# Performance work log

Measured on AMD Instinct MI355X. Metric: run time of the kernel, lower is better.

Reference implementation:

```python
import jax, jax.numpy as jnp
import numpy as np

N_NODES = 50000
N_EDGES = 800000
N_REL = 8
OUT_CH = 64      # latent dim of z
HID = 128        # hidden_channels
IN_CH = 128      # reconstructed feature dim
NEG_SLOPE = 0.2


def rgat_conv(x, src, dst, edge_type, weight, q, k, bias, num_nodes):
    """PyG RGATConv, heads=1, dim=1, additive-self-attention, across-relation.
    x: [N, in]; weight: [R, in, out]; q,k: [out, 1]; bias: [out]."""
    # per-relation transform of all nodes, then per-edge gather (same math as
    # per-edge bmm with weight[edge_type], avoids [E, in, out] intermediate)
    x_all = jnp.einsum('ni,rio->nro', x, weight)          # [N, R, out]
    x_j = x_all[src, edge_type]                            # [E, out]
    x_i = x_all[dst, edge_type]                            # [E, out]
    alpha = (x_i @ q + x_j @ k)[:, 0]                      # [E]
    alpha = jax.nn.leaky_relu(alpha, NEG_SLOPE)
    # scatter-softmax over destination neighborhoods
    m = jax.ops.segment_max(alpha, dst, num_segments=num_nodes)
    m = jnp.where(jnp.isfinite(m), m, 0.0)                 # empty segments -> 0
    ex = jnp.exp(alpha - m[dst])
    denom = jax.ops.segment_sum(ex, dst, num_segments=num_nodes)
    a = ex / (denom[dst] + 1e-16)                          # [E]
    out = jax.ops.segment_sum(a[:, None] * x_j, dst, num_segments=num_nodes)
    return out + bias


def setup_inputs() -> dict:
    key = jax.random.key(0)
    ks = jax.random.split(key, 12)
    z = jax.random.normal(ks[0], (N_NODES, OUT_CH), dtype=jnp.float32)
    edge_index = jax.random.randint(ks[1], (2, N_EDGES), 0, N_NODES, dtype=jnp.int32)
    edge_type = jax.random.randint(ks[2], (N_EDGES,), 0, N_REL, dtype=jnp.int32)

    def glorot(k_, shape):
        fan = shape[-2] + shape[-1]
        return jax.random.normal(k_, shape, dtype=jnp.float32) * jnp.sqrt(2.0 / fan)

    return {
        'z': z,
        'lin_w': glorot(ks[3], (HID, OUT_CH)),
        'lin_b': jnp.zeros((HID,), dtype=jnp.float32),
        'w1': glorot(ks[4], (N_REL, HID, HID)),
        'q1': glorot(ks[5], (HID, 1)),
        'k1': glorot(ks[6], (HID, 1)),
        'b1': jnp.zeros((HID,), dtype=jnp.float32),
        'w2': glorot(ks[7], (N_REL, HID, IN_CH)),
        'q2': glorot(ks[8], (IN_CH, 1)),
        'k2': glorot(ks[9], (IN_CH, 1)),
        'b2': jnp.zeros((IN_CH,), dtype=jnp.float32),
        'edge_index': edge_index,
        'edge_type': edge_type,
    }


def reference(z, lin_w, lin_b, w1, q1, k1, b1, w2, q2, k2, b2, edge_index, edge_type):
    num_nodes = z.shape[0]
    src, dst = edge_index[0], edge_index[1]
    h = z @ lin_w.T + lin_b                                 # nn.Linear
    h = jax.nn.relu(rgat_conv(h, src, dst, edge_type, w1, q1, k1, b1, num_nodes))
    # dropout is identity in eval mode
    recon_x = rgat_conv(h, src, dst, edge_type, w2, q2, k2, b2, num_nodes)
    return recon_x
```

## Files before the change

### kernel.cpp

```cpp
#include <hip/hip_runtime.h>
#include <hip/hip_bf16.h>
#include <cstdint>
#include <cstddef>

#define N_NODES 50000
#define N_EDGES 800000
#define NSEG    (N_NODES * 8)

using frag_t = __attribute__((ext_vector_type(8))) short;
using f32x4  = __attribute__((ext_vector_type(4))) float;

__device__ __forceinline__ short f2bf(float x) {
    __hip_bfloat16 h = __float2bfloat16(x);
    return *reinterpret_cast<short*>(&h);
}
__device__ __forceinline__ float bf2f(unsigned int u) {
    union { unsigned int i; float f; } v;
    v.i = u << 16;
    return v.f;
}
__device__ __forceinline__ unsigned int packbf2(float lo, float hi) {
    unsigned int a = (unsigned short)f2bf(lo);
    unsigned int b = (unsigned short)f2bf(hi);
    return a | (b << 16);
}


__global__ void hist_kernel(const int* __restrict__ dst, const int* __restrict__ et,
                            int* __restrict__ deg8, int E) {
    int e = blockIdx.x * 256 + threadIdx.x;
    if (e < E) atomicAdd(&deg8[dst[e] * 8 + et[e]], 1);
}

__global__ __launch_bounds__(256) void scan_part(const int* __restrict__ deg8,
                                                 int* __restrict__ part, int M) {
    __shared__ int red[256];
    int t = threadIdx.x;
    int idx = blockIdx.x * 1024 + t * 4;
    int s = 0;
    if (idx + 3 < M) {
        int4 d = *(const int4*)(deg8 + idx);
        s = d.x + d.y + d.z + d.w;
    } else {
        for (int c = 0; c < 4; c++) if (idx + c < M) s += deg8[idx + c];
    }
    red[t] = s;
    __syncthreads();
    #pragma unroll
    for (int off = 128; off; off >>= 1) {
        if (t < off) red[t] += red[t + off];
        __syncthreads();
    }
    if (t == 0) part[blockIdx.x] = red[0];
}

__global__ __launch_bounds__(512) void scan_mid(int* __restrict__ part, int nparts,
                                                int* __restrict__ rowp, int M) {
    __shared__ int buf[512];
    int t = threadIdx.x;
    int own = (t < nparts) ? part[t] : 0;
    buf[t] = own;
    __syncthreads();
    for (int off = 1; off < 512; off <<= 1) {
        int v = buf[t];
        int u = (t >= off) ? buf[t - off] : 0;
        __syncthreads();
        buf[t] = v + u;
        __syncthreads();
    }
    if (t < nparts) part[t] = buf[t] - own;
    if (t == 511) rowp[M] = buf[511];
}

__global__ __launch_bounds__(256) void scan_fix(const int* __restrict__ deg8,
                                                const int* __restrict__ part,
                                                int* __restrict__ rowp,
                                                int* __restrict__ cursor, int M) {
    __shared__ int wsum[4];
    int t = threadIdx.x, lane = t & 63, w = t >> 6;
    int idx = blockIdx.x * 1024 + t * 4;
    int v0 = 0, v1 = 0, v2 = 0, v3 = 0;
    if (idx + 3 < M) {
        int4 d = *(const int4*)(deg8 + idx);
        v0 = d.x; v1 = d.y; v2 = d.z; v3 = d.w;
    } else {
        if (idx     < M) v0 = deg8[idx];
        if (idx + 1 < M) v1 = deg8[idx + 1];
        if (idx + 2 < M) v2 = deg8[idx + 2];
        if (idx + 3 < M) v3 = deg8[idx + 3];
    }
    int tsum = v0 + v1 + v2 + v3;
    int sc = tsum;
    #pragma unroll
    for (int off = 1; off < 64; off <<= 1) {
        int u = __shfl_up(sc, off, 64);
        if (lane >= off) sc += u;
    }
    if (lane == 63) wsum[w] = sc;
    __syncthreads();
    int woff = 0;
    for (int i = 0; i < w; i++) woff += wsum[i];
    int excl = part[blockIdx.x] + woff + sc - tsum;
    if (idx     < M) { rowp[idx]     = excl; cursor[idx]     = excl; } excl += v0;
    if (idx + 1 < M) { rowp[idx + 1] = excl; cursor[idx + 1] = excl; } excl += v1;
    if (idx + 2 < M) { rowp[idx + 2] = excl; cursor[idx + 2] = excl; } excl += v2;
    if (idx + 3 < M) { rowp[idx + 3] = excl; cursor[idx + 3] = excl; }
}

__global__ void fill_kernel(const int* __restrict__ src, const int* __restrict__ dst,
                            const int* __restrict__ et, int* __restrict__ cursor,
                            int* __restrict__ sorted, int E) {
    int e = blockIdx.x * 256 + threadIdx.x;
    if (e < E) {
        int pos = atomicAdd(&cursor[dst[e] * 8 + et[e]], 1);
        sorted[pos] = src[e] | (et[e] << 16);
    }
}


__global__ __launch_bounds__(256) void gemm_lin(const float* __restrict__ A,
                                                const float* __restrict__ B,
                                                const float* __restrict__ bias,
                                                unsigned short* __restrict__ hb, int N) {
    const int Kdim = 64;
    __shared__ float As[32][64];
    __shared__ float Bs[32][128];
    int t = threadIdx.x;
    int n0 = blockIdx.x * 64;
    int rg = t >> 4, cg = t & 15;
    int an = t >> 2, ak = (t & 3) * 8;
    float acc[4][8] = {};

    for (int k0 = 0; k0 < Kdim; k0 += 32) {
        int gn = n0 + an;
        if (gn < N) {
            const float* ap = A + (size_t)gn * Kdim + k0 + ak;
            float4 v0 = *(const float4*)ap;
            float4 v1 = *(const float4*)(ap + 4);
            As[ak + 0][an] = v0.x; As[ak + 1][an] = v0.y;
            As[ak + 2][an] = v0.z; As[ak + 3][an] = v0.w;
            As[ak + 4][an] = v1.x; As[ak + 5][an] = v1.y;
            As[ak + 6][an] = v1.z; As[ak + 7][an] = v1.w;
        } else {
            #pragma unroll
            for (int c = 0; c < 8; c++) As[ak + c][an] = 0.f;
        }
        {
            int o = t >> 1, kh = (t & 1) * 16;
            const float* bp = B + (size_t)o * Kdim + k0 + kh;
            #pragma unroll
            for (int j = 0; j < 4; j++) {
                float4 v = ((const float4*)bp)[j];
                Bs[kh + j * 4 + 0][o] = v.x;
                Bs[kh + j * 4 + 1][o] = v.y;
                Bs[kh + j * 4 + 2][o] = v.z;
                Bs[kh + j * 4 + 3][o] = v.w;
            }
        }
        __syncthreads();
        #pragma unroll
        for (int k = 0; k < 32; k++) {
            float a[4], b[8];
            *(float4*)&a[0] = *(const float4*)&As[k][rg * 4];
            *(float4*)&b[0] = *(const float4*)&Bs[k][cg * 8];
            *(float4*)&b[4] = *(const float4*)&Bs[k][cg * 8 + 4];
            #pragma unroll
            for (int i = 0; i < 4; i++)
                #pragma unroll
                for (int j = 0; j < 8; j++)
                    acc[i][j] = fmaf(a[i], b[j], acc[i][j]);
        }
        __syncthreads();
    }
    #pragma unroll
    for (int i = 0; i < 4; i++) {
        int gn = n0 + rg * 4 + i;
        if (gn < N) {
            unsigned short us[8];
            #pragma unroll
            for (int j = 0; j < 8; j++)
                us[j] = (unsigned short)f2bf(acc[i][j] + bias[cg * 8 + j]);
            *(int4*)(hb + (size_t)gn * 128 + cg * 8) = *(int4*)&us[0];
        }
    }
}


__global__ void wconv_kernel(const float* __restrict__ W, short* __restrict__ Bf) {
    int idx = blockIdx.x * 256 + threadIdx.x;
    int k = idx >> 7, o = idx & 127;
    float v = W[(size_t)k * 128 + o];
    Bf[(((size_t)(k >> 3) * 128) + o) * 8 + (k & 7)] = f2bf(v);
}


__global__ void wqk_kernel(const float* __restrict__ W, const float* __restrict__ q,
                           const float* __restrict__ k, float* __restrict__ wq,
                           float* __restrict__ wk) {
    int g = blockIdx.x * 256 + threadIdx.x;
    int which = g >> 10;
    int r = (g >> 7) & 7;
    int i = g & 127;
    const float* vec = which ? k : q;
    const float* wrow = W + ((size_t)r * 128 + i) * 128;
    float acc = 0.f;
    #pragma unroll 4
    for (int o = 0; o < 128; o++) acc = fmaf(wrow[o], vec[o], acc);
    (which ? wk : wq)[r * 128 + i] = acc;
}


__global__ __launch_bounds__(256) void qk_table_kernel(const unsigned short* __restrict__ xb,
                                                       const float* __restrict__ wq,
                                                       const float* __restrict__ wk,
                                                       float* __restrict__ Q,
                                                       float* __restrict__ K, int N) {
    int n = blockIdx.x * 256 + threadIdx.x;
    if (n >= N) return;
    const uint2* row = (const uint2*)(xb + (size_t)n * 128);
    float aq[8] = {}, ak[8] = {};
    for (int i = 0; i < 32; i++) {
        uint2 d = row[i];
        float x0 = bf2f(d.x & 0xFFFFu);
        float x1 = bf2f(d.x >> 16);
        float x2 = bf2f(d.y & 0xFFFFu);
        float x3 = bf2f(d.y >> 16);
        int c = i * 4;
        #pragma unroll
        for (int r = 0; r < 8; r++) {
            const float* wqr = wq + r * 128 + c;
            const float* wkr = wk + r * 128 + c;
            aq[r] = fmaf(x0, wqr[0], fmaf(x1, wqr[1], fmaf(x2, wqr[2], fmaf(x3, wqr[3], aq[r]))));
            ak[r] = fmaf(x0, wkr[0], fmaf(x1, wkr[1], fmaf(x2, wkr[2], fmaf(x3, wkr[3], ak[r]))));
        }
    }
    float4* qp = (float4*)(Q + (size_t)n * 8);
    qp[0] = *(float4*)&aq[0];
    qp[1] = *(float4*)&aq[4];
    float4* kp = (float4*)(K + (size_t)n * 8);
    kp[0] = *(float4*)&ak[0];
    kp[1] = *(float4*)&ak[4];
}


__global__ __launch_bounds__(256) void agg_s_kernel(const unsigned short* __restrict__ hb,
                                                    const float* __restrict__ Q,
                                                    const float* __restrict__ Kt,
                                                    const int* __restrict__ rowp8,
                                                    const int* __restrict__ sorted,
                                                    short* __restrict__ s, int N) {
    int wv = threadIdx.x >> 6;
    int lane = threadIdx.x & 63;
    int n = blockIdx.x * 4 + wv;
    if (n >= N) return;
    int beg = rowp8[n * 8];
    int end = rowp8[n * 8 + 8];
    int deg = end - beg;
    unsigned int* spw = (unsigned int*)(s + (size_t)n * 1024);
    const unsigned int* hbu = (const unsigned int*)hb;

    if (deg == 0) {
        int4 z = {0, 0, 0, 0};
        int4* p = (int4*)spw;
        p[lane * 2]     = z;
        p[lane * 2 + 1] = z;
        return;
    }

    float2 acc = {0.f, 0.f};
    int rcur = 0;

    if (deg <= 64) {
        int pk = 0;
        float a = -INFINITY;
        if (lane < deg) {
            pk = sorted[beg + lane];
            int srcn = pk & 0xFFFF, etj = pk >> 16;
            a = Q[(size_t)n * 8 + etj] + Kt[(size_t)srcn * 8 + etj];
            a = (a > 0.f) ? a : 0.2f * a;
        }
        float m = a;
        #pragma unroll
        for (int off = 32; off; off >>= 1) m = fmaxf(m, __shfl_xor(m, off, 64));
        float e = (lane < deg) ? __expf(a - m) : 0.f;
        float sum = e;
        #pragma unroll
        for (int off = 32; off; off >>= 1) sum += __shfl_xor(sum, off, 64);
        float w = e / (sum + 1e-16f);

        int j = 0;
        for (; j + 4 <= deg; j += 4) {
            int   p0 = __shfl(pk, j, 64),     p1 = __shfl(pk, j + 1, 64);
            int   p2 = __shfl(pk, j + 2, 64), p3 = __shfl(pk, j + 3, 64);
            float w0 = __shfl(w, j, 64),      w1 = __shfl(w, j + 1, 64);
            float w2 = __shfl(w, j + 2, 64),  w3 = __shfl(w, j + 3, 64);
            unsigned int d0 = hbu[(size_t)(p0 & 0xFFFF) * 64 + lane];
            unsigned int d1 = hbu[(size_t)(p1 & 0xFFFF) * 64 + lane];
            unsigned int d2 = hbu[(size_t)(p2 & 0xFFFF) * 64 + lane];
            unsigned int d3 = hbu[(size_t)(p3 & 0xFFFF) * 64 + lane];
            int e0 = p0 >> 16, e1 = p1 >> 16, e2 = p2 >> 16, e3 = p3 >> 16;
            while (rcur < e0) { spw[rcur * 64 + lane] = packbf2(acc.x, acc.y); acc.x = acc.y = 0.f; rcur++; }
            acc.x = fmaf(w0, bf2f(d0 & 0xFFFF), acc.x); acc.y = fmaf(w0, bf2f(d0 >> 16), acc.y);
            while (rcur < e1) { spw[rcur * 64 + lane] = packbf2(acc.x, acc.y); acc.x = acc.y = 0.f; rcur++; }
            acc.x = fmaf(w1, bf2f(d1 & 0xFFFF), acc.x); acc.y = fmaf(w1, bf2f(d1 >> 16), acc.y);
            while (rcur < e2) { spw[rcur * 64 + lane] = packbf2(acc.x, acc.y); acc.x = acc.y = 0.f; rcur++; }
            acc.x = fmaf(w2, bf2f(d2 & 0xFFFF), acc.x); acc.y = fmaf(w2, bf2f(d2 >> 16), acc.y);
            while (rcur < e3) { spw[rcur * 64 + lane] = packbf2(acc.x, acc.y); acc.x = acc.y = 0.f; rcur++; }
            acc.x = fmaf(w3, bf2f(d3 & 0xFFFF), acc.x); acc.y = fmaf(w3, bf2f(d3 >> 16), acc.y);
        }
        for (; j < deg; j++) {
            int   p0 = __shfl(pk, j, 64);
            float w0 = __shfl(w, j, 64);
            unsigned int d0 = hbu[(size_t)(p0 & 0xFFFF) * 64 + lane];
            int e0 = p0 >> 16;
            while (rcur < e0) { spw[rcur * 64 + lane] = packbf2(acc.x, acc.y); acc.x = acc.y = 0.f; rcur++; }
            acc.x = fmaf(w0, bf2f(d0 & 0xFFFF), acc.x); acc.y = fmaf(w0, bf2f(d0 >> 16), acc.y);
        }
        while (rcur < 8) { spw[rcur * 64 + lane] = packbf2(acc.x, acc.y); acc.x = acc.y = 0.f; rcur++; }
        return;
    }

    auto logit = [&](int j) -> float {
        int pk = sorted[beg + j];
        int srcn = pk & 0xFFFF, etj = pk >> 16;
        float a = Q[(size_t)n * 8 + etj] + Kt[(size_t)srcn * 8 + etj];
        return (a > 0.f) ? a : 0.2f * a;
    };
    float m = -INFINITY;
    for (int j = lane; j < deg; j += 64) m = fmaxf(m, logit(j));
    #pragma unroll
    for (int off = 32; off; off >>= 1) m = fmaxf(m, __shfl_xor(m, off, 64));
    float sum = 0.f;
    for (int j = lane; j < deg; j += 64) sum += __expf(logit(j) - m);
    #pragma unroll
    for (int off = 32; off; off >>= 1) sum += __shfl_xor(sum, off, 64);
    float inv = 1.f / (sum + 1e-16f);

    for (int j0 = 0; j0 < deg; j0 += 64) {
        int cnt = min(64, deg - j0);
        int pk = 0;
        float w = 0.f;
        if (lane < cnt) {
            pk = sorted[beg + j0 + lane];
            int srcn = pk & 0xFFFF, etj = pk >> 16;
            float a = Q[(size_t)n * 8 + etj] + Kt[(size_t)srcn * 8 + etj];
            a = (a > 0.f) ? a : 0.2f * a;
            w = __expf(a - m) * inv;
        }
        for (int j = 0; j < cnt; j++) {
            int   p0 = __shfl(pk, j, 64);
            float w0 = __shfl(w, j, 64);
            unsigned int d0 = hbu[(size_t)(p0 & 0xFFFF) * 64 + lane];
            int e0 = p0 >> 16;
            while (rcur < e0) { spw[rcur * 64 + lane] = packbf2(acc.x, acc.y); acc.x = acc.y = 0.f; rcur++; }
            acc.x = fmaf(w0, bf2f(d0 & 0xFFFF), acc.x); acc.y = fmaf(w0, bf2f(d0 >> 16), acc.y);
        }
    }
    while (rcur < 8) { spw[rcur * 64 + lane] = packbf2(acc.x, acc.y); acc.x = acc.y = 0.f; rcur++; }
}


__global__ __launch_bounds__(256) void gemm_mfma(const short* __restrict__ s,
                                                 const short* __restrict__ Bf,
                                                 const float* __restrict__ bias,
                                                 float* __restrict__ Cout,
                                                 unsigned short* __restrict__ hbout,
                                                 int N, int relu) {
    __shared__ short As[4096];
    __shared__ short Bs[4096];
    int t = threadIdx.x;
    int w = t >> 6, lane = t & 63;
    int lhi = lane >> 4, llo = lane & 15;
    int n0 = blockIdx.x * 128;
    int arow = t >> 1, ahalf = t & 1;
    int agn = n0 + arow;
    const short* arp = s + (size_t)agn * 1024 + ahalf * 16;
    short* adst = As + ((ahalf * 2) * 128 + arow) * 8;
    f32x4 acc[16] = {};

    for (int c = 0; c < 32; c++) {
        int4 a0v = {0, 0, 0, 0}, a1v = {0, 0, 0, 0};
        if (agn < N) {
            const int4* ap = (const int4*)(arp + c * 32);
            a0v = ap[0];
            a1v = ap[1];
        }
        *(int4*)adst              = a0v;
        *(int4*)(adst + 128 * 8)  = a1v;
        {
            const short* spb = Bf + (size_t)c * 4096 + t * 16;
            short* dp = Bs + t * 16;
            *(int4*)dp       = *(const int4*)spb;
            *(int4*)(dp + 8) = *(const int4*)(spb + 8);
        }
        __syncthreads();
        frag_t a0 = *(const frag_t*)(As + ((size_t)lhi * 128 + w * 32 + llo) * 8);
        frag_t a1 = *(const frag_t*)(As + ((size_t)lhi * 128 + w * 32 + llo + 16) * 8);
        #pragma unroll
        for (int ct = 0; ct < 8; ct++) {
            frag_t b = *(const frag_t*)(Bs + ((size_t)lhi * 128 + ct * 16 + llo) * 8);
            acc[ct]     = __builtin_amdgcn_mfma_f32_16x16x32_bf16(a0, b, acc[ct], 0, 0, 0);
            acc[8 + ct] = __builtin_amdgcn_mfma_f32_16x16x32_bf16(a1, b, acc[8 + ct], 0, 0, 0);
        }
        __syncthreads();
    }
    #pragma unroll
    for (int rt = 0; rt < 2; rt++) {
        #pragma unroll
        for (int ct = 0; ct < 8; ct++) {
            int col = ct * 16 + llo;
            float bv = bias[col];
            #pragma unroll
            for (int rg = 0; rg < 4; rg++) {
                int rown = n0 + w * 32 + rt * 16 + lhi * 4 + rg;
                if (rown < N) {
                    float v = acc[rt * 8 + ct][rg] + bv;
                    if (relu) v = fmaxf(v, 0.f);
                    if (Cout)  Cout[(size_t)rown * 128 + col] = v;
                    if (hbout) hbout[(size_t)rown * 128 + col] = (unsigned short)f2bf(v);
                }
            }
        }
    }
}


extern "C" void kernel_launch(void* const* d_in, const int* in_sizes, int n_in,
                              void* d_out, int out_size, void* d_ws, size_t ws_size,
                              hipStream_t stream) {
    const float* z     = (const float*)d_in[0];
    const float* lin_w = (const float*)d_in[1];
    const float* lin_b = (const float*)d_in[2];
    const float* w1    = (const float*)d_in[3];
    const float* q1    = (const float*)d_in[4];
    const float* k1    = (const float*)d_in[5];
    const float* b1    = (const float*)d_in[6];
    const float* w2    = (const float*)d_in[7];
    const float* q2    = (const float*)d_in[8];
    const float* k2    = (const float*)d_in[9];
    const float* b2    = (const float*)d_in[10];
    const int*   ei    = (const int*)d_in[11];
    const int*   et    = (const int*)d_in[12];
    float* out = (float*)d_out;

    char* ws = (char*)d_ws;
    size_t off = 0;
    auto alloc = [&](size_t bytes) -> void* {
        void* p = ws + off;
        off += (bytes + 255) & ~(size_t)255;
        return p;
    };
    short* s     = (short*)alloc((size_t)N_NODES * 1024 * 2);
    unsigned short* hb = (unsigned short*)alloc((size_t)N_NODES * 128 * 2);
    float* Q     = (float*)alloc((size_t)N_NODES * 8 * 4);
    float* K     = (float*)alloc((size_t)N_NODES * 8 * 4);
    int* sorted  = (int*)alloc((size_t)N_EDGES * 4);
    int* deg8    = (int*)alloc((size_t)NSEG * 4);
    int* rowp8   = (int*)alloc((size_t)(NSEG + 1) * 4);
    int* cursor8 = (int*)alloc((size_t)NSEG * 4);
    int* part    = (int*)alloc(1024 * 4);
    float* wq    = (float*)alloc(8 * 128 * 4);
    float* wk    = (float*)alloc(8 * 128 * 4);
    short* Bf    = (short*)alloc((size_t)1024 * 128 * 2);

    const int* src = ei;
    const int* dst = ei + N_EDGES;

    const int M = NSEG;
    const int nparts = (M + 1023) / 1024;

    hipMemsetAsync(deg8, 0, (size_t)M * 4, stream);
    hist_kernel<<<(N_EDGES + 255) / 256, 256, 0, stream>>>(dst, et, deg8, N_EDGES);
    scan_part<<<nparts, 256, 0, stream>>>(deg8, part, M);
    scan_mid<<<1, 512, 0, stream>>>(part, nparts, rowp8, M);
    scan_fix<<<nparts, 256, 0, stream>>>(deg8, part, rowp8, cursor8, M);
    fill_kernel<<<(N_EDGES + 255) / 256, 256, 0, stream>>>(src, dst, et, cursor8, sorted, N_EDGES);

    gemm_lin<<<(N_NODES + 63) / 64, 256, 0, stream>>>(z, lin_w, lin_b, hb, N_NODES);

    int mgrid = (N_NODES + 127) / 128;
    int agrid = (N_NODES + 3) / 4;
    int qgrid = (N_NODES + 255) / 256;

    wconv_kernel<<<512, 256, 0, stream>>>(w1, Bf);
    wqk_kernel<<<8, 256, 0, stream>>>(w1, q1, k1, wq, wk);
    qk_table_kernel<<<qgrid, 256, 0, stream>>>(hb, wq, wk, Q, K, N_NODES);
    agg_s_kernel<<<agrid, 256, 0, stream>>>(hb, Q, K, rowp8, sorted, s, N_NODES);
    gemm_mfma<<<mgrid, 256, 0, stream>>>(s, Bf, b1, (float*)nullptr, hb, N_NODES, 1);

    wconv_kernel<<<512, 256, 0, stream>>>(w2, Bf);
    wqk_kernel<<<8, 256, 0, stream>>>(w2, q2, k2, wq, wk);
    qk_table_kernel<<<qgrid, 256, 0, stream>>>(hb, wq, wk, Q, K, N_NODES);
    agg_s_kernel<<<agrid, 256, 0, stream>>>(hb, Q, K, rowp8, sorted, s, N_NODES);
    gemm_mfma<<<mgrid, 256, 0, stream>>>(s, Bf, b2, out, (unsigned short*)nullptr, N_NODES, 0);
}
```

Before: 414.9 us.

## Merge weight-prep kernels, deepen gather unroll, use direct global-to-LDS loads in GEMM

Fuses the weight bf16 conversion and the W·q/W·k precompute into one launch, which removes a launch per layer. The aggregation inner loop is unrolled to 8 edges so more gathers are in flight at once. The MFMA GEMM now stages its A and B tiles with global_load_lds, which skips the register round trip. The GEMM no longer bounds-checks rows past N on the last block, so it may read past the end of s unless the buffer is padded.

After: 411.3 us. No clear change (-0.9%).

```diff
diff --git a/kernel.cpp b/kernel.cpp
--- a/kernel.cpp
+++ b/kernel.cpp
@@ -9,6 +9,9 @@
 
 using frag_t = __attribute__((ext_vector_type(8))) short;
 using f32x4  = __attribute__((ext_vector_type(4))) float;
+
+typedef const __attribute__((address_space(1))) void* gptr_t;
+typedef __attribute__((address_space(3))) void* lptr_t;
 
 __device__ __forceinline__ short f2bf(float x) {
     __hip_bfloat16 h = __float2bfloat16(x);
@@ -186,27 +189,28 @@
 }
 
 
-__global__ void wconv_kernel(const float* __restrict__ W, short* __restrict__ Bf) {
-    int idx = blockIdx.x * 256 + threadIdx.x;
-    int k = idx >> 7, o = idx & 127;
-    float v = W[(size_t)k * 128 + o];
-    Bf[(((size_t)(k >> 3) * 128) + o) * 8 + (k & 7)] = f2bf(v);
-}
-
-
-__global__ void wqk_kernel(const float* __restrict__ W, const float* __restrict__ q,
-                           const float* __restrict__ k, float* __restrict__ wq,
-                           float* __restrict__ wk) {
+__global__ void wprep_kernel(const float* __restrict__ W, const float* __restrict__ q,
+                             const float* __restrict__ k, short* __restrict__ Bf,
+                             float* __restrict__ wq, float* __restrict__ wk) {
     int g = blockIdx.x * 256 + threadIdx.x;
-    int which = g >> 10;
-    int r = (g >> 7) & 7;
-    int i = g & 127;
-    const float* vec = which ? k : q;
-    const float* wrow = W + ((size_t)r * 128 + i) * 128;
-    float acc = 0.f;
-    #pragma unroll 4
-    for (int o = 0; o < 128; o++) acc = fmaf(wrow[o], vec[o], acc);
-    (which ? wk : wq)[r * 128 + i] = acc;
+    if (g < 131072) {
+        int kk = g >> 7, o = g & 127;
+        float v = W[(size_t)kk * 128 + o];
+        Bf[(((size_t)(kk >> 3) * 128) + o) * 8 + (kk & 7)] = f2bf(v);
+        return;
+    }
+    int h = g - 131072;
+    if (h < 2048) {
+        int which = h >> 10;
+        int r = (h >> 7) & 7;
+        int i = h & 127;
+        const float* vec = which ? k : q;
+        const float* wrow = W + ((size_t)r * 128 + i) * 128;
+        float acc = 0.f;
+        #pragma unroll 4
+        for (int o = 0; o < 128; o++) acc = fmaf(wrow[o], vec[o], acc);
+        (which ? wk : wq)[r * 128 + i] = acc;
+    }
 }
 
 
@@ -289,24 +293,23 @@
         float w = e / (sum + 1e-16f);
 
         int j = 0;
-        for (; j + 4 <= deg; j += 4) {
-            int   p0 = __shfl(pk, j, 64),     p1 = __shfl(pk, j + 1, 64);
-            int   p2 = __shfl(pk, j + 2, 64), p3 = __shfl(pk, j + 3, 64);
-            float w0 = __shfl(w, j, 64),      w1 = __shfl(w, j + 1, 64);
-            float w2 = __shfl(w, j + 2, 64),  w3 = __shfl(w, j + 3, 64);
-            unsigned int d0 = hbu[(size_t)(p0 & 0xFFFF) * 64 + lane];
-            unsigned int d1 = hbu[(size_t)(p1 & 0xFFFF) * 64 + lane];
-            unsigned int d2 = hbu[(size_t)(p2 & 0xFFFF) * 64 + lane];
-            unsigned int d3 = hbu[(size_t)(p3 & 0xFFFF) * 64 + lane];
-            int e0 = p0 >> 16, e1 = p1 >> 16, e2 = p2 >> 16, e3 = p3 >> 16;
-            while (rcur < e0) { spw[rcur * 64 + lane] = packbf2(acc.x, acc.y); acc.x = acc.y = 0.f; rcur++; }
-            acc.x = fmaf(w0, bf2f(d0 & 0xFFFF), acc.x); acc.y = fmaf(w0, bf2f(d0 >> 16), acc.y);
-            while (rcur < e1) { spw[rcur * 64 + lane] = packbf2(acc.x, acc.y); acc.x = acc.y = 0.f; rcur++; }
-            acc.x = fmaf(w1, bf2f(d1 & 0xFFFF), acc.x); acc.y = fmaf(w1, bf2f(d1 >> 16), acc.y);
-            while (rcur < e2) { spw[rcur * 64 + lane] = packbf2(acc.x, acc.y); acc.x = acc.y = 0.f; rcur++; }
-            acc.x = fmaf(w2, bf2f(d2 & 0xFFFF), acc.x); acc.y = fmaf(w2, bf2f(d2 >> 16), acc.y);
-            while (rcur < e3) { spw[rcur * 64 + lane] = packbf2(acc.x, acc.y); acc.x = acc.y = 0.f; rcur++; }
-            acc.x = fmaf(w3, bf2f(d3 & 0xFFFF), acc.x); acc.y = fmaf(w3, bf2f(d3 >> 16), acc.y);
+        for (; j + 8 <= deg; j += 8) {
+            int pp[8]; float ww[8]; unsigned int dd[8];
+            #pragma unroll
+            for (int i = 0; i < 8; i++) {
+                pp[i] = __shfl(pk, j + i, 64);
+                ww[i] = __shfl(w,  j + i, 64);
+            }
+            #pragma unroll
+            for (int i = 0; i < 8; i++)
+                dd[i] = hbu[(size_t)(pp[i] & 0xFFFF) * 64 + lane];
+            #pragma unroll
+            for (int i = 0; i < 8; i++) {
+                int e0 = pp[i] >> 16;
+                while (rcur < e0) { spw[rcur * 64 + lane] = packbf2(acc.x, acc.y); acc.x = acc.y = 0.f; rcur++; }
+                acc.x = fmaf(ww[i], bf2f(dd[i] & 0xFFFF), acc.x);
+                acc.y = fmaf(ww[i], bf2f(dd[i] >> 16),    acc.y);
+            }
         }
         for (; j < deg; j++) {
             int   p0 = __shfl(pk, j, 64);
@@ -314,7 +317,8 @@
             unsigned int d0 = hbu[(size_t)(p0 & 0xFFFF) * 64 + lane];
             int e0 = p0 >> 16;
             while (rcur < e0) { spw[rcur * 64 + lane] = packbf2(acc.x, acc.y); acc.x = acc.y = 0.f; rcur++; }
-            acc.x = fmaf(w0, bf2f(d0 & 0xFFFF), acc.x); acc.y = fmaf(w0, bf2f(d0 >> 16), acc.y);
+            acc.x = fmaf(w0, bf2f(d0 & 0xFFFF), acc.x);
+            acc.y = fmaf(w0, bf2f(d0 >> 16),    acc.y);
         }
         while (rcur < 8) { spw[rcur * 64 + lane] = packbf2(acc.x, acc.y); acc.x = acc.y = 0.f; rcur++; }
         return;
@@ -353,7 +357,8 @@
             unsigned int d0 = hbu[(size_t)(p0 & 0xFFFF) * 64 + lane];
             int e0 = p0 >> 16;
             while (rcur < e0) { spw[rcur * 64 + lane] = packbf2(acc.x, acc.y); acc.x = acc.y = 0.f; rcur++; }
-            acc.x = fmaf(w0, bf2f(d0 & 0xFFFF), acc.x); acc.y = fmaf(w0, bf2f(d0 >> 16), acc.y);
+            acc.x = fmaf(w0, bf2f(d0 & 0xFFFF), acc.x);
+            acc.y = fmaf(w0, bf2f(d0 >> 16),    acc.y);
         }
     }
     while (rcur < 8) { spw[rcur * 64 + lane] = packbf2(acc.x, acc.y); acc.x = acc.y = 0.f; rcur++; }
@@ -372,26 +377,23 @@
     int w = t >> 6, lane = t & 63;
     int lhi = lane >> 4, llo = lane & 15;
     int n0 = blockIdx.x * 128;
-    int arow = t >> 1, ahalf = t & 1;
-    int agn = n0 + arow;
-    const short* arp = s + (size_t)agn * 1024 + ahalf * 16;
-    short* adst = As + ((ahalf * 2) * 128 + arow) * 8;
+    const char* sB = (const char*)s;
+    const char* bB = (const char*)Bf;
     f32x4 acc[16] = {};
 
     for (int c = 0; c < 32; c++) {
-        int4 a0v = {0, 0, 0, 0}, a1v = {0, 0, 0, 0};
-        if (agn < N) {
-            const int4* ap = (const int4*)(arp + c * 32);
-            a0v = ap[0];
-            a1v = ap[1];
-        }
-        *(int4*)adst              = a0v;
-        *(int4*)(adst + 128 * 8)  = a1v;
-        {
-            const short* spb = Bf + (size_t)c * 4096 + t * 16;
-            short* dp = Bs + t * 16;
-            *(int4*)dp       = *(const int4*)spb;
-            *(int4*)(dp + 8) = *(const int4*)(spb + 8);
+        #pragma unroll
+        for (int i = 0; i < 2; i++) {
+            int row = i * 64 + lane;
+            const void* gp = sB + (size_t)(n0 + row) * 2048 + c * 64 + w * 16;
+            __builtin_amdgcn_global_load_lds(
+                (gptr_t)gp, (lptr_t)((char*)As + w * 2048 + i * 1024), 16, 0, 0);
+        }
+        #pragma unroll
+        for (int i = 0; i < 2; i++) {
+            const void* gp = bB + (size_t)c * 8192 + w * 2048 + i * 1024 + lane * 16;
+            __builtin_amdgcn_global_load_lds(
+                (gptr_t)gp, (lptr_t)((char*)Bs + w * 2048 + i * 1024), 16, 0, 0);
         }
         __syncthreads();
         frag_t a0 = *(const frag_t*)(As + ((size_t)lhi * 128 + w * 32 + llo) * 8);
@@ -481,15 +483,14 @@
     int mgrid = (N_NODES + 127) / 128;
     int agrid = (N_NODES + 3) / 4;
     int qgrid = (N_NODES + 255) / 256;
-
-    wconv_kernel<<<512, 256, 0, stream>>>(w1, Bf);
-    wqk_kernel<<<8, 256, 0, stream>>>(w1, q1, k1, wq, wk);
+    int wgrid = (131072 + 2048) / 256;
+
+    wprep_kernel<<<wgrid, 256, 0, stream>>>(w1, q1, k1, Bf, wq, wk);
     qk_table_kernel<<<qgrid, 256, 0, stream>>>(hb, wq, wk, Q, K, N_NODES);
     agg_s_kernel<<<agrid, 256, 0, stream>>>(hb, Q, K, rowp8, sorted, s, N_NODES);
     gemm_mfma<<<mgrid, 256, 0, stream>>>(s, Bf, b1, (float*)nullptr, hb, N_NODES, 1);
 
-    wconv_kernel<<<512, 256, 0, stream>>>(w2, Bf);
-    wqk_kernel<<<8, 256, 0, stream>>>(w2, q2, k2, wq, wk);
+    wprep_kernel<<<wgrid, 256, 0, stream>>>(w2, q2, k2, Bf, wq, wk);
     qk_table_kernel<<<qgrid, 256, 0, stream>>>(hb, wq, wk, Q, K, N_NODES);
     agg_s_kernel<<<agrid, 256, 0, stream>>>(hb, Q, K, rowp8, sorted, s, N_NODES);
     gemm_mfma<<<mgrid, 256, 0, stream>>>(s, Bf, b2, out, (unsigned short*)nullptr, N_NODES, 0);
```
